# Performance work log

Measured on AMD Instinct MI355X. Metric: run time of the kernel, lower is better.

## Reference

```python
import jax, jax.numpy as jnp
import numpy as np

D = 1024          # feature dim (x_dim)
C = 32            # n classes (way)
SHOTS = 32
N_SUP = C * SHOTS
Q = 1024
REG = 0.5         # reg_param


def setup_inputs() -> dict:
    key = jax.random.key(0)
    ks = jax.random.split(key, 5)
    support_x = jax.random.normal(ks[0], (N_SUP, D), dtype=jnp.float32)
    query_x = jax.random.normal(ks[1], (Q, D), dtype=jnp.float32)
    labels_idx = (jnp.arange(N_SUP, dtype=jnp.int32) % C)  # every class present, equal shots
    m = jax.random.normal(ks[2], (1, D), dtype=jnp.float32) * 0.01
    kappa = jnp.float32(0.1)
    nu = jnp.float32(D)
    triu_diag = jnp.ones((D,), dtype=jnp.float32)
    triu_lower = jnp.eye(D, dtype=jnp.float32) + 0.01 * jax.random.normal(ks[3], (D, D), dtype=jnp.float32)
    return {"support_x": support_x, "query_x": query_x, "labels_idx": labels_idx,
            "m": m, "kappa": kappa, "nu": nu,
            "triu_diag": triu_diag, "triu_lower": triu_lower}


def _metaqda_fb(support_x, query_x, labels_idx, m, kappa, nu, triu_diag, triu_lower):
    onehot = jax.nn.one_hot(labels_idx, C, dtype=support_x.dtype)      # [N, C]
    Nj = jnp.sum(onehot, axis=0)                                       # [C]
    kappa_ = jnp.abs(kappa) + 1e-6
    nu_ = jnp.maximum(nu, jnp.float32(D - 1 + 1e-6))

    # Cholesky-factor prior scatter matrix: L @ L^T
    lower_mask = jnp.tril(jnp.ones((D, D), dtype=support_x.dtype), k=-1)
    L = jnp.diag(jnp.abs(triu_diag)) + triu_lower * lower_mask
    prior_S = L @ L.T                                                  # [D, D]

    # per-class sums (replaces python loop of rank-1 outer products with GEMMs)
    sum_x = onehot.T @ support_x                                       # [C, D]
    mean_x = sum_x / Nj[:, None]
    # sum_n x x^T per class: contract through [N,C,D] intermediate
    SXX = jnp.einsum('nc,nd,ne->cde', onehot, support_x, support_x)    # [C, D, D]

    kN = kappa_ + Nj                                                   # [C]
    mu = (kappa_ / kN)[:, None] * m + (Nj / kN)[:, None] * mean_x      # [C, D]

    mm = m.T @ m                                                       # [D, D]  (self_outer of [1,D])
    mumu = jnp.einsum('cd,ce->cde', mu, mu)                            # [C, D, D]
    S = prior_S[None] + SXX + kappa_ * mm[None] - kN[:, None, None] * mumu

    scale = (kN + 1.0) / ((nu_ + Nj - D + 1.0) * kN)                   # [C]
    sigma = S * scale[:, None, None]                                   # [C, D, D]

    sigma_inv = (1.0 - REG) * jnp.linalg.inv(sigma) + REG * jnp.eye(D, dtype=sigma.dtype)

    common = nu_ + Nj + 1.0 - D                                        # [C]
    _, logdet = jnp.linalg.slogdet(sigma)
    bias = (jax.lax.lgamma(0.5 * (common + D)) - jax.lax.lgamma(0.5 * common)
            - 0.5 * D * jnp.log(common) - 0.5 * logdet)                # [C]

    diff = query_x[:, None, :] - mu[None, :, :]                        # [Q, C, D]
    dist = jnp.einsum('qcd,cde,qce->qc', diff, sigma_inv, diff)        # [Q, C]
    preds = bias[None, :] - 0.5 * (common + D)[None, :] * jnp.log1p(dist / common[None, :])
    return preds


def reference(support_x, query_x, labels_idx, m, kappa, nu, triu_diag, triu_lower):
    return _metaqda_fb(support_x, query_x, labels_idx, m, kappa, nu, triu_diag, triu_lower)
```

## Files before the change

### kernel.cpp

```cpp
#include <hip/hip_runtime.h>
#include <math.h>

#define Dk 1024
#define Ck 32
#define Nk 1024
#define Qk 1024
#define REGP 0.5f
#define NB 64
#define NROWSV (Qk + Nk + Ck + 1)

#define CO_KAPPA 0
#define CO_NU    1
#define CO_NJ    2
#define CO_KN    34
#define CO_SCALE 66
#define CO_COMMON 98
#define CO_COEF  130
#define CO_BIASA 162
#define CO_BIASF 200

#define O_P    0u
#define O_W    2162688u
#define O_T    3211264u
#define O_MU   3473408u
#define O_QM   3506176u
#define O_MB   3538944u
#define O_MI   3578112u
#define O_QNY  3617280u
#define O_QNO  3618304u
#define O_MUN  3619328u
#define O_GMM  3619360u
#define O_EX   3619392u
#define O_CONS 3619408u
#define O_CIDX 3619664u
#define O_YH   3652432u
#define O_YM   4733776u
#define O_YL   5815120u
#define O_WH   6896464u
#define O_WM   7420752u
#define O_WL   7945040u
#define O_OH   8469328u
#define O_OM   9550672u
#define O_OL   10632016u

#define WS_DECL \
    float* P     = Wbuf + O_P;    (void)P; \
    float* W     = Wbuf + O_W;    (void)W; \
    float* Tb    = Wbuf + O_T;    (void)Tb; \
    float* QM    = Wbuf + O_QM;   (void)QM; \
    float* Mbuf  = Wbuf + O_MB;   (void)Mbuf; \
    float* Minv  = Wbuf + O_MI;   (void)Minv; \
    float* qny   = Wbuf + O_QNY;  (void)qny; \
    float* qno   = Wbuf + O_QNO;  (void)qno; \
    float* mun2o = Wbuf + O_MUN;  (void)mun2o; \
    float* gmm   = Wbuf + O_GMM;  (void)gmm; \
    float* extraf= Wbuf + O_EX;   (void)extraf; \
    float* cons  = Wbuf + O_CONS; (void)cons; \
    int*   cidx  = (int*)(Wbuf + O_CIDX); (void)cidx; \
    ushort* sYh = (ushort*)(Wbuf + O_YH); (void)sYh; \
    ushort* sYm = (ushort*)(Wbuf + O_YM); (void)sYm; \
    ushort* sYl = (ushort*)(Wbuf + O_YL); (void)sYl; \
    ushort* sWh = (ushort*)(Wbuf + O_WH); (void)sWh; \
    ushort* sWm = (ushort*)(Wbuf + O_WM); (void)sWm; \
    ushort* sWl = (ushort*)(Wbuf + O_WL); (void)sWl; \
    ushort* sOh = (ushort*)(Wbuf + O_OH); (void)sOh; \
    ushort* sOm = (ushort*)(Wbuf + O_OM); (void)sOm; \
    ushort* sOl = (ushort*)(Wbuf + O_OL); (void)sOl;

typedef __attribute__((ext_vector_type(8))) __bf16 bf16x8;
typedef __attribute__((ext_vector_type(4))) float f32x4;

#define MFMA(a, b, c) __builtin_amdgcn_mfma_f32_16x16x32_bf16(a, b, c, 0, 0, 0)

__device__ __forceinline__ ushort f2bf(float x) {
    unsigned u = __float_as_uint(x);
    return (ushort)((u + 0x7FFFu + ((u >> 16) & 1u)) >> 16);
}
__device__ __forceinline__ float bf2f(ushort h) {
    return __uint_as_float(((unsigned)h) << 16);
}
__device__ __forceinline__ void split1(float x, ushort& h, ushort& m, ushort& l) {
    h = f2bf(x);
    float r1 = x - bf2f(h);
    m = f2bf(r1);
    l = f2bf(r1 - bf2f(m));
}
__device__ __forceinline__ void split_store4(ushort* ph, ushort* pm, ushort* pl,
                                             size_t o, float4 v) {
    float vv[4] = {v.x, v.y, v.z, v.w};
    ushort4 H, M, L;
    ushort* Hp = (ushort*)&H; ushort* Mp = (ushort*)&M; ushort* Lp = (ushort*)&L;
#pragma unroll
    for (int c = 0; c < 4; ++c) split1(vv[c], Hp[c], Mp[c], Lp[c]);
    *(ushort4*)(ph + o) = H;
    *(ushort4*)(pm + o) = M;
    *(ushort4*)(pl + o) = L;
}

__device__ __forceinline__ float wave_red(float s) {
#pragma unroll
    for (int o = 32; o > 0; o >>= 1) s += __shfl_down(s, o, 64);
    return s;
}

#define LDSA(c, r, k8) ((c) * 5120 + (r) * 40 + (k8))
#define LDSB(c, r, k8) (15360 + (c) * 2560 + (r) * 40 + (k8))
#define LDS_HW 23040

__device__ __forceinline__ void tile_fetch8(
    bf16x8* ra, bf16x8* rb,
    const ushort* Ah, const ushort* Am, const ushort* Al, int aRow0, int aRowMax,
    const ushort* Bh, const ushort* Bm, const ushort* Bl, int bRow0,
    int kcol, int t)
{
    bf16x8 z = {};
    int row = t >> 2, kg = t & 3;
#pragma unroll
    for (int u = 0; u < 3; ++u) {
        const ushort* As = (u == 0) ? Ah : ((u == 1) ? Am : Al);
        int gr = aRow0 + row;
        ra[u] = (gr < aRowMax) ? *(const bf16x8*)(As + (size_t)gr * 1024 + kcol + kg * 8) : z;
    }
#pragma unroll
    for (int u = 0; u < 2; ++u) {
        int slot = t + u * 512;
        if (slot < 768) {
            int comp = slot >> 8, rem = slot & 255;
            int br = rem >> 2, bkg = rem & 3;
            const ushort* Bs = (comp == 0) ? Bh : ((comp == 1) ? Bm : Bl);
            rb[u] = *(const bf16x8*)(Bs + (size_t)(bRow0 + br) * 1024 + kcol + bkg * 8);
        }
    }
}

__device__ __forceinline__ void tile_store8(ushort* lds, const bf16x8* ra, const bf16x8* rb, int t) {
    int row = t >> 2, kg = t & 3;
#pragma unroll
    for (int u = 0; u < 3; ++u)
        *(bf16x8*)(lds + LDSA(u, row, kg * 8)) = ra[u];
#pragma unroll
    for (int u = 0; u < 2; ++u) {
        int slot = t + u * 512;
        if (slot < 768) {
            int comp = slot >> 8, rem = slot & 255;
            int br = rem >> 2, bkg = rem & 3;
            *(bf16x8*)(lds + LDSB(comp, br, bkg * 8)) = rb[u];
        }
    }
}

__device__ __forceinline__ void tile_compute8(const ushort* lds, f32x4 acc[4],
                                              int w, int lr, int lk) {
    bf16x8 af[3], bf_[4][3];
#pragma unroll
    for (int c = 0; c < 3; ++c)
        af[c] = *(const bf16x8*)(lds + LDSA(c, w * 16 + lr, lk * 8));
#pragma unroll
    for (int cf = 0; cf < 4; ++cf)
#pragma unroll
        for (int c = 0; c < 3; ++c)
            bf_[cf][c] = *(const bf16x8*)(lds + LDSB(c, cf * 16 + lr, lk * 8));
#pragma unroll
    for (int cf = 0; cf < 4; ++cf) {
        f32x4 a = acc[cf];
        a = MFMA(af[0], bf_[cf][0], a);
        a = MFMA(af[0], bf_[cf][1], a);
        a = MFMA(af[1], bf_[cf][0], a);
        a = MFMA(af[0], bf_[cf][2], a);
        a = MFMA(af[2], bf_[cf][0], a);
        a = MFMA(af[1], bf_[cf][1], a);
        acc[cf] = a;
    }
}

__device__ __forceinline__ void tile_gemm8(
    ushort* lds, f32x4 acc[4],
    const ushort* Ah, const ushort* Am, const ushort* Al, int aRow0, int aRowMax,
    const ushort* Bh, const ushort* Bm, const ushort* Bl, int bRow0,
    int kbase, int ksteps, int t)
{
    const int w = t >> 6, lr = t & 15, lk = (t >> 4) & 3;
    bf16x8 ra[3], rb[2];
    tile_fetch8(ra, rb, Ah, Am, Al, aRow0, aRowMax, Bh, Bm, Bl, bRow0, kbase * 32, t);
    tile_store8(lds, ra, rb, t);
    __syncthreads();
    for (int kt = 0; kt < ksteps; ++kt) {
        if (kt + 1 < ksteps)
            tile_fetch8(ra, rb, Ah, Am, Al, aRow0, aRowMax, Bh, Bm, Bl, bRow0,
                        (kbase + kt + 1) * 32, t);
        tile_compute8(lds, acc, w, lr, lk);
        __syncthreads();
        if (kt + 1 < ksteps)
            tile_store8(lds, ra, rb, t);
        __syncthreads();
    }
}

__device__ __forceinline__ void fetch4(float4* reg, const float* src, int ld,
                                       int rowbase, int rowmax, int colbase, int t) {
#pragma unroll
    for (int u = 0; u < 4; ++u) {
        int slot = t + u * 256;
        int r = slot >> 4, c4 = slot & 15;
        int gr = rowbase + r;
        reg[u] = (gr < rowmax) ? *(const float4*)(src + (size_t)gr * ld + colbase + c4 * 4)
                               : make_float4(0.f, 0.f, 0.f, 0.f);
    }
}
__device__ __forceinline__ void stT(float* dst, const float4* reg, int t) {
#pragma unroll
    for (int u = 0; u < 4; ++u) {
        int slot = t + u * 256;
        int r = slot >> 4, c4 = slot & 15;
        dst[(c4 * 4 + 0) * 68 + r] = reg[u].x;
        dst[(c4 * 4 + 1) * 68 + r] = reg[u].y;
        dst[(c4 * 4 + 2) * 68 + r] = reg[u].z;
        dst[(c4 * 4 + 3) * 68 + r] = reg[u].w;
    }
}
__device__ __forceinline__ void stN(float* dst, const float4* reg, int t) {
#pragma unroll
    for (int u = 0; u < 4; ++u) {
        int slot = t + u * 256;
        int r = slot >> 4, c4 = slot & 15;
        *(float4*)(dst + r * 68 + c4 * 4) = reg[u];
    }
}
__device__ __forceinline__ void gemm16(const float* At, const float* Bt,
                                       float acc[4][4], int tx, int ty) {
#pragma unroll 4
    for (int kk = 0; kk < NB; ++kk) {
        float4 a = *(const float4*)(At + kk * 68 + ty * 4);
        float4 b = *(const float4*)(Bt + kk * 68 + tx * 4);
        float av[4] = {a.x, a.y, a.z, a.w};
        float bv[4] = {b.x, b.y, b.z, b.w};
#pragma unroll
        for (int r = 0; r < 4; ++r)
#pragma unroll
            for (int s = 0; s < 4; ++s) acc[r][s] += av[r] * bv[s];
    }
}
__device__ __forceinline__ void mm_task(
    const float* aSrc, int aLd, int aRow, int aRowMax, int aCol, int aRowStep, int aColStep,
    const float* bSrc, int bLd, int bRow, int bRowMax, int bCol, int bRowStep, int bColStep,
    bool bTrans, int k0, int k1,
    float acc[4][4], float* smA, float* smB, int t, int tx, int ty)
{
    float4 ra[4], rb[4];
    fetch4(ra, aSrc, aLd, aRow + k0 * aRowStep, aRowMax, aCol + k0 * aColStep, t);
    fetch4(rb, bSrc, bLd, bRow + k0 * bRowStep, bRowMax, bCol + k0 * bColStep, t);
    stT(smA, ra, t);
    if (bTrans) stT(smB, rb, t); else stN(smB, rb, t);
    __syncthreads();
    for (int kt = k0; kt < k1; ++kt) {
        if (kt + 1 < k1) {
            fetch4(ra, aSrc, aLd, aRow + (kt + 1) * aRowStep, aRowMax, aCol + (kt + 1) * aColStep, t);
            fetch4(rb, bSrc, bLd, bRow + (kt + 1) * bRowStep, bRowMax, bCol + (kt + 1) * bColStep, t);
        }
        gemm16(smA, smB, acc, tx, ty);
        __syncthreads();
        if (kt + 1 < k1) {
            stT(smA, ra, t);
            if (bTrans) stT(smB, rb, t); else stN(smB, rb, t);
        }
        __syncthreads();
    }
}

__global__ __launch_bounds__(256) void k_p0(const float* qx, const int* labels,
                                            const float* mvec, const float* kappa,
                                            const float* nu, const float* td,
                                            const float* tl, float* Wbuf) {
    __shared__ __align__(16) float smem[9216];
    float* smA = smem;
    float* sX  = smem + 8704;
    WS_DECL
    const int t = threadIdx.x;
    const int lane = t & 63, wv = t >> 6;
    const int tau = blockIdx.x;

    if (tau == 0) {
        int* scnt = (int*)sX;
        if (t < Ck) scnt[t] = 0;
        __syncthreads();
        for (int n = t; n < Nk; n += 256) {
            int l = labels[n];
            int pos = atomicAdd(&scnt[l], 1);
            cidx[l * Nk + pos] = n;
        }
        __syncthreads();
        if (t < Ck) {
            float kap = fabsf(kappa[0]) + 1e-6f;
            float nu_ = fmaxf(nu[0], (float)(Dk - 1) + 1e-6f);
            float Njf = (float)scnt[t];
            float kN = kap + Njf;
            if (t == 0) { cons[CO_KAPPA] = kap; cons[CO_NU] = nu_; }
            cons[CO_NJ + t] = Njf;
            cons[CO_KN + t] = kN;
            cons[CO_SCALE + t] = (kN + 1.0f) / ((nu_ + Njf - (float)Dk + 1.0f) * kN);
            float common = nu_ + Njf + 1.0f - (float)Dk;
            cons[CO_COMMON + t] = common;
            cons[CO_COEF + t] = 0.5f * (common + (float)Dk);
            cons[CO_BIASA + t] = lgammaf(0.5f * (common + (float)Dk)) - lgammaf(0.5f * common)
                                 - 0.5f * (float)Dk * logf(common);
        }
    } else if (tau == 1) {
        float s = 0.f;
        for (int i = t; i < Dk; i += 256) s += logf(fabsf(td[i]));
        s = wave_red(s);
        if (lane == 0) sX[wv] = s;
        __syncthreads();
        if (t == 0) extraf[0] = 2.f * (sX[0] + sX[1] + sX[2] + sX[3]);
    } else if (tau < 18) {
        int b0 = (tau - 2) * NB;
        for (int idx = t; idx < 64 * 64; idx += 256) {
            int m = idx >> 6, i = idx & 63;
            smem[i * 72 + m] = (m > i) ? tl[(size_t)(b0 + m) * Dk + b0 + i] : 0.f;
        }
        if (t < 64) smem[4608 + t] = 1.f / fabsf(td[b0 + t]);
        __syncthreads();
        if (t < 64) {
            const int j = t;
            float r[64];
#pragma unroll
            for (int m = 0; m < 64; ++m) r[m] = (m == j) ? 1.f : 0.f;
#pragma unroll
            for (int i = 0; i < 64; ++i) {
                float x = r[i] * smem[4608 + i];
                r[i] = x;
#pragma unroll
                for (int g = (i >> 2); g < 16; ++g) {
                    float4 lt = *(const float4*)&smem[i * 72 + g * 4];
                    r[g * 4 + 0] -= lt.x * x;
                    r[g * 4 + 1] -= lt.y * x;
                    r[g * 4 + 2] -= lt.z * x;
                    r[g * 4 + 3] -= lt.w * x;
                }
            }
#pragma unroll
            for (int i = 0; i < 64; ++i)
                W[(size_t)(b0 + i) * Dk + b0 + j] = r[i];
        }
    } else if (tau < 21) {
        int base = (tau - 18) * 13056;
        for (int i = t; i < 13056 && base + i < 39168; i += 256) Mbuf[base + i] = 0.f;
    } else if (tau == 21) {
        if (t < 32) { mun2o[t] = 0.f; gmm[t] = 0.f; }
    } else if (tau < 86) {
        int rbase = (tau - 22) * 16;
        for (int j = wv; j < 16; j += 4) {
            const float* row = qx + (size_t)(rbase + j) * Dk;
            float s = 0.f;
            for (int d = lane; d < Dk; d += 64) { float v = row[d]; s += v * v; }
            s = wave_red(s);
            if (lane == 0) qno[rbase + j] = s;
        }
    } else if (tau < 150) {
        int rbase = (tau - 86) * 16;
        for (int j = 0; j < 16; ++j) {
            int r = rbase + j;
            float4 v = ((const float4*)(qx + (size_t)r * Dk))[t];
            split_store4(sYh, sYm, sYl, (size_t)r * 1024 + (size_t)t * 4, v);
        }
    } else if (tau == 150) {
        float4 v = ((const float4*)mvec)[t];
        split_store4(sYh, sYm, sYl, (size_t)2080 * 1024 + (size_t)t * 4, v);
    } else {
        int rbase = (tau - 151) * 16;
        for (int j = 0; j < 16; ++j)
            ((float4*)(P + (size_t)(rbase + j) * 1024))[t] = make_float4(0, 0, 0, 0);
    }
}

__global__ __launch_bounds__(256) void k_p1(const float* sx, const float* mvec, float* Wbuf) {
    __shared__ float sX[512];
    WS_DECL
    const int t = threadIdx.x;
    const int lane = t & 63, wv = t >> 6;
    const int tau = blockIdx.x;
    if (tau < 128) {
        int c = tau >> 2;
        int d = ((tau & 3) << 8) + t;
        int Nj = (int)cons[CO_NJ + c];
        float kap = cons[CO_KAPPA], kN = cons[CO_KN + c];
        float acc = 0.f;
        for (int s = 0; s < Nj; ++s) acc += sx[(size_t)cidx[c * Nk + s] * Dk + d];
        float muv = (kap * mvec[d] + acc) / kN;
        size_t o = (size_t)(2048 + c) * 1024 + d;
        ushort h, m_, l_;
        split1(muv, h, m_, l_);
        sYh[o] = h; sYm[o] = m_; sYl[o] = l_;
        float s2 = wave_red(muv * muv);
        if (lane == 0) sX[wv] = s2;
        __syncthreads();
        if (t == 0) atomicAdd(&mun2o[c], sX[0] + sX[1] + sX[2] + sX[3]);
    } else {
        int rbase = (tau - 128) * 16;
        for (int j = 0; j < 16; ++j) {
            int n = rbase + j;
            int srcrow = cidx[(n >> 5) * Nk + (n & 31)];
            float4 v = ((const float4*)(sx + (size_t)srcrow * Dk))[t];
            split_store4(sYh, sYm, sYl, (size_t)(1024 + n) * 1024 + (size_t)t * 4, v);
        }
    }
}

__global__ __launch_bounds__(256) void k_t1(const float* tl, float* Wbuf) {
    __shared__ __align__(16) float smem[8704];
    float* smA = smem;
    float* smB = smem + 4352;
    WS_DECL
    const int t = threadIdx.x;
    const int tx = t & 15, ty = t >> 4;
    const int BIG = 1 << 30;
    int pb = blockIdx.x * 128;
    float acc[4][4] = {};
    mm_task(tl, Dk, pb + 64, BIG, pb, 0, NB,
            W, Dk, pb, BIG, pb, NB, 0, false, 0, 1,
            acc, smA, smB, t, tx, ty);
    {
        float4 ra[4];
        fetch4(ra, W, Dk, pb + 64, BIG, pb + 64, t);
#pragma unroll
        for (int r = 0; r < 4; ++r)
#pragma unroll
            for (int s = 0; s < 4; ++s)
                smB[(ty * 4 + r) * 68 + tx * 4 + s] = acc[r][s];
        stT(smA, ra, t);
    }
    __syncthreads();
    float acc2[4][4] = {};
    gemm16(smA, smB, acc2, tx, ty);
    __syncthreads();
#pragma unroll
    for (int r = 0; r < 4; ++r)
#pragma unroll
        for (int s = 0; s < 4; ++s)
            W[(size_t)(pb + 64 + ty * 4 + r) * Dk + pb + tx * 4 + s] = -acc2[r][s];
}

__global__ __launch_bounds__(256) void k_tr_a(const float* tl, float* Wbuf, int h, int ht) {
    __shared__ __align__(16) float smem[8704];
    float* smA = smem;
    float* smB = smem + 4352;
    WS_DECL
    const int t = threadIdx.x;
    const int tx = t & 15, ty = t >> 4;
    const int BIG = 1 << 30;
    int tau = blockIdx.x;
    int p = tau / (ht * ht), rr = tau % (ht * ht);
    int i = rr / ht, j = rr % ht;
    int pb = p * 2 * h;
    float acc[4][4] = {};
    mm_task(tl, Dk, pb + h + i * NB, BIG, pb, 0, NB,
            W, Dk, pb, BIG, pb + j * NB, NB, 0, false, 0, ht,
            acc, smA, smB, t, tx, ty);
    float* Tp = Tb + (size_t)p * h * h;
#pragma unroll
    for (int r = 0; r < 4; ++r)
#pragma unroll
        for (int s = 0; s < 4; ++s)
            Tp[(size_t)(i * NB + ty * 4 + r) * h + j * NB + tx * 4 + s] = acc[r][s];
}

__global__ __launch_bounds__(256) void k_tr_b(float* Wbuf, int h, int ht) {
    __shared__ __align__(16) float smem[8704];
    float* smA = smem;
    float* smB = smem + 4352;
    WS_DECL
    const int t = threadIdx.x;
    const int tx = t & 15, ty = t >> 4;
    const int BIG = 1 << 30;
    int tau = blockIdx.x;
    int p = tau / (ht * ht), rr = tau % (ht * ht);
    int i = rr / ht, j = rr % ht;
    int pb = p * 2 * h;
    const float* Tp = Tb + (size_t)p * h * h;
    float acc[4][4] = {};
    mm_task(W, Dk, pb + h + i * NB, BIG, pb + h, 0, NB,
            Tp, h, 0, BIG, j * NB, NB, 0, false, 0, ht,
            acc, smA, smB, t, tx, ty);
#pragma unroll
    for (int r = 0; r < 4; ++r)
#pragma unroll
        for (int s = 0; s < 4; ++s)
            W[(size_t)(pb + h + i * NB + ty * 4 + r) * Dk + pb + j * NB + tx * 4 + s] = -acc[r][s];
}

__global__ __launch_bounds__(256) void k_cvtw(float* Wbuf) {
    WS_DECL
    const int t = threadIdx.x;
#pragma unroll
    for (int u = 0; u < 4; ++u) {
        unsigned g = blockIdx.x * 1024u + u * 256u + t;
        float4 v = ((const float4*)W)[g];
        split_store4(sWh, sWm, sWl, (size_t)g * 4, v);
    }
}

__global__ __launch_bounds__(512) void k_yg(float* Wbuf) {
    __shared__ __align__(16) ushort lds[LDS_HW];
    WS_DECL
    const int t = threadIdx.x;
    int b = blockIdx.x;
    int s = (b & 7) * 34 + (b >> 3);
    int jt = 15 - s / 17, rt = s % 17;
    f32x4 acc[4] = {};
    tile_gemm8(lds, acc, sYh, sYm, sYl, rt * 128, 2081,
               sWh, sWm, sWl, jt * 64, 0, (jt + 1) * 2, t);
    const int w = t >> 6, lr = t & 15, lk = (t >> 4) & 3;
#pragma unroll
    for (int cf = 0; cf < 4; ++cf)
#pragma unroll
        for (int r = 0; r < 4; ++r) {
            int grow = rt * 128 + w * 16 + lk * 4 + r;
            if (grow < NROWSV) {
                size_t o = (size_t)grow * 1024 + jt * 64 + cf * 16 + lr;
                ushort h, m_, l_;
                split1(acc[cf][r], h, m_, l_);
                sOh[o] = h; sOm[o] = m_; sOl[o] = l_;
            }
        }
}

__global__ __launch_bounds__(512) void k_p4m(float* Wbuf) {
    __shared__ __align__(16) ushort lds[LDS_HW];
    WS_DECL
    const int t = threadIdx.x;
    int b = blockIdx.x;
    int s = (b & 7) * 74 + (b >> 3);
    const int w = t >> 6, lr = t & 15, lk = (t >> 4) & 3;
    f32x4 acc[4] = {};
    if (s < 576) {
        int qt = s / 36, rem = s % 36;
        int mt = rem >> 2, kc = rem & 3;
        tile_gemm8(lds, acc, sOh, sOm, sOl, 1024 + mt * 128, 2081,
                   sOh, sOm, sOl, qt * 64, kc * 8, 8, t);
#pragma unroll
        for (int cf = 0; cf < 4; ++cf)
#pragma unroll
            for (int r = 0; r < 4; ++r) {
                int n = mt * 128 + w * 16 + lk * 4 + r;
                if (n < Nk + Ck + 1)
                    atomicAdd(&P[(size_t)n * 1024 + qt * 64 + cf * 16 + lr], acc[cf][r]);
            }
    } else {
        int qt = s - 576;
        tile_gemm8(lds, acc, sYh, sYm, sYl, 2048, 2081,
                   sYh, sYm, sYl, qt * 64, 0, 32, t);
#pragma unroll
        for (int cf = 0; cf < 4; ++cf)
#pragma unroll
            for (int r = 0; r < 4; ++r) {
                int rq = w * 16 + lk * 4 + r;
                if (rq < 32)
                    QM[(size_t)rq * 1024 + qt * 64 + cf * 16 + lr] = acc[cf][r];
            }
    }
}

__global__ __launch_bounds__(256) void k_gram(float* Wbuf) {
    __shared__ __align__(16) float smA[34 * 68];
    WS_DECL
    const int t = threadIdx.x;
    const int lane = t & 63, wv = t >> 6;
    const int tau = blockIdx.x;
    if (tau < 128) {
        int c = tau >> 2, kc = tau & 3;
        float accg[5];
        int iu[5], ju[5];
#pragma unroll
        for (int u = 0; u < 5; ++u) {
            int e = t + u * 256;
            iu[u] = e / 34; ju[u] = e - iu[u] * 34;
            accg[u] = 0.f;
        }
        for (int kt = kc * 4; kt < kc * 4 + 4; ++kt) {
            for (int e2 = t; e2 < 34 * NB; e2 += 256) {
                int i = e2 >> 6, k = e2 & 63;
                int yr = (i < 32) ? (Qk + c * 32 + i) : ((i == 32) ? (Qk + Nk + c) : (Qk + Nk + Ck));
                size_t o = (size_t)yr * 1024 + kt * NB + k;
                smA[i * 68 + k] = bf2f(sOh[o]) + bf2f(sOm[o]) + bf2f(sOl[o]);
            }
            __syncthreads();
#pragma unroll
            for (int u = 0; u < 5; ++u) {
                int e = t + u * 256;
                if (e < 1156) {
                    float s = 0.f;
                    for (int k = 0; k < NB; ++k) s += smA[iu[u] * 68 + k] * smA[ju[u] * 68 + k];
                    accg[u] += s;
                }
            }
            __syncthreads();
        }
#pragma unroll
        for (int u = 0; u < 5; ++u) {
            int e = t + u * 256;
            if (e < 1156)
                atomicAdd(&Mbuf[c * 1224 + iu[u] * 36 + ju[u]], accg[u]);
        }
    } else {
        int rbase = (tau - 128) * 16;
        for (int j = wv; j < 16; j += 4) {
            size_t ro = (size_t)(rbase + j) * 1024;
            float s = 0.f;
            for (int d = lane; d < Dk; d += 64) {
                size_t o = ro + d;
                float v = bf2f(sOh[o]) + bf2f(sOm[o]) + bf2f(sOl[o]);
                s += v * v;
            }
            s = wave_red(s);
            if (lane == 0) qny[rbase + j] = s;
        }
    }
}

__global__ __launch_bounds__(256) void k_p5(float* Wbuf) {
    __shared__ float smem[2464];
    float* Ml = smem;
    float* Z  = smem + 1200;
    float* Dv = smem + 2400;
    WS_DECL
    const int t = threadIdx.x;
    const int c = blockIdx.x;
    float kN = cons[CO_KN + c], kap = cons[CO_KAPPA];
    for (int e = t; e < 34 * 34; e += 256) {
        int i = e / 34, j = e - i * 34;
        Ml[i * 35 + j] = Mbuf[c * 1224 + i * 36 + j];
    }
    __syncthreads();
    if (t == 0) {
        gmm[c] = Ml[32 * 35 + 32];
        Ml[32 * 35 + 32] += -1.f / kN;
        Ml[33 * 35 + 33] += 1.f / kap;
    }
    if (t < 32) Ml[t * 35 + t] += 1.f;
    __syncthreads();
    for (int j = 0; j < 34; ++j) {
        if (t == 0) {
            float s = Ml[j * 35 + j];
            for (int k = 0; k < j; ++k) s -= Ml[j * 35 + k] * Ml[j * 35 + k] * Dv[k];
            Dv[j] = s;
        }
        __syncthreads();
        if (t > j && t < 34) {
            float s = Ml[t * 35 + j];
            for (int k = 0; k < j; ++k) s -= Ml[t * 35 + k] * Ml[j * 35 + k] * Dv[k];
            Ml[t * 35 + j] = s / Dv[j];
        }
        __syncthreads();
    }
    if (t < 34) {
        for (int i = 0; i < 34; ++i) {
            float s = (i == t) ? 1.f : 0.f;
            for (int k = 0; k < i; ++k) s -= Ml[i * 35 + k] * Z[k * 35 + t];
            Z[i * 35 + t] = s;
        }
        for (int i = 33; i >= 0; --i) {
            float s = Z[i * 35 + t] / Dv[i];
            for (int k = i + 1; k < 34; ++k) s -= Ml[k * 35 + i] * Z[k * 35 + t];
            Z[i * 35 + t] = s;
        }
    }
    __syncthreads();
    for (int e = t; e < 34 * 34; e += 256) {
        int i = e / 34, j = e - i * 34;
        Minv[c * 1224 + i * 36 + j] = Z[i * 35 + j];
    }
    if (t == 0) {
        float ld = 0.f;
        for (int j = 0; j < 34; ++j) ld += logf(fabsf(Dv[j]));
        float scale = cons[CO_SCALE + c];
        float logdet = (float)Dk * logf(scale) + extraf[0] + logf(kN) + logf(kap) + ld;
        cons[CO_BIASF + c] = cons[CO_BIASA + c] - 0.5f * logdet;
    }
}

__global__ __launch_bounds__(256) void k_p6(float* Wbuf, float* out) {
    __shared__ __align__(16) float smem[3904];
    float* Mi  = smem;
    float* wL  = smem + 1200;
    float* gsm = smem + 3520;
    float* red = smem + 3520 + 128;
    WS_DECL
    const int t = threadIdx.x;
    const int tau = blockIdx.x;
    int qt = tau >> 5, c = tau & 31;
    for (int e = t; e < 34 * 34; e += 256) {
        int i = e / 34, j = e - i * 34;
        Mi[i * 35 + j] = Minv[c * 1224 + i * 36 + j];
    }
    if (t < 34)
        gsm[t] = (t < 32) ? Mbuf[c * 1224 + t * 36 + 32]
                          : ((t == 32) ? gmm[c] : Mbuf[c * 1224 + 33 * 36 + 32]);
    __syncthreads();
    for (int e = t; e < 34 * NB; e += 256) {
        int i = e >> 6, qq = e & 63;
        int prow = (i < 32) ? (c * 32 + i) : ((i == 32) ? (Nk + c) : (Nk + Ck));
        wL[i * 68 + qq] = P[(size_t)prow * Qk + qt * NB + qq] - gsm[i];
    }
    __syncthreads();
    {
        int q = t & 63, part = t >> 6;
        int start = (part < 2) ? part * 9 : 18 + (part - 2) * 8;
        int cnt = (part < 2) ? 9 : 8;
        float partial = 0.f;
        for (int i = start; i < start + cnt; ++i) {
            float v = 0.f;
            for (int j = 0; j < 34; ++j) v += Mi[i * 35 + j] * wL[j * 68 + q];
            partial += v * wL[i * 68 + q];
        }
        red[part * 64 + q] = partial;
    }
    __syncthreads();
    if (t < 64) {
        int q = t;
        float quad = red[q] + red[64 + q] + red[128 + q] + red[192 + q];
        int qg = qt * NB + q;
        float w32 = wL[32 * 68 + q];
        float ydist2 = qny[qg] - 2.f * w32 - gmm[c];
        float dd = qno[qg] + mun2o[c] - 2.f * QM[(size_t)c * Qk + qg];
        float scale = cons[CO_SCALE + c], common = cons[CO_COMMON + c];
        float dist = (1.f - REGP) / scale * (ydist2 - quad) + REGP * dd;
        out[(size_t)qg * Ck + c] = cons[CO_BIASF + c] - cons[CO_COEF + c] * log1pf(dist / common);
    }
}

extern "C" void kernel_launch(void* const* d_in, const int* in_sizes, int n_in,
                              void* d_out, int out_size, void* d_ws, size_t ws_size,
                              hipStream_t stream) {
    const float* sx = (const float*)d_in[0];
    const float* qx = (const float*)d_in[1];
    const int* labels = (const int*)d_in[2];
    const float* mvec = (const float*)d_in[3];
    const float* kappa = (const float*)d_in[4];
    const float* nu = (const float*)d_in[5];
    const float* td = (const float*)d_in[6];
    const float* tl = (const float*)d_in[7];
    float* W = (float*)d_ws;
    float* out = (float*)d_out;

    hipLaunchKernelGGL(k_p0, dim3(219), dim3(256), 0, stream,
                       qx, labels, mvec, kappa, nu, td, tl, W);
    hipLaunchKernelGGL(k_p1, dim3(192), dim3(256), 0, stream, sx, mvec, W);
    hipLaunchKernelGGL(k_t1, dim3(8), dim3(256), 0, stream, tl, W);
    for (int l = 2; l <= 4; ++l) {
        int h = 32 << l, ht = h >> 6, pairs = 16 >> l;
        int nt = pairs * ht * ht;
        hipLaunchKernelGGL(k_tr_a, dim3(nt), dim3(256), 0, stream, tl, W, h, ht);
        hipLaunchKernelGGL(k_tr_b, dim3(nt), dim3(256), 0, stream, W, h, ht);
    }
    hipLaunchKernelGGL(k_cvtw, dim3(256), dim3(256), 0, stream, W);
    hipLaunchKernelGGL(k_yg, dim3(272), dim3(512), 0, stream, W);
    hipLaunchKernelGGL(k_p4m, dim3(592), dim3(512), 0, stream, W);
    hipLaunchKernelGGL(k_gram, dim3(192), dim3(256), 0, stream, W);
    hipLaunchKernelGGL(k_p5, dim3(32), dim3(256), 0, stream, W);
    hipLaunchKernelGGL(k_p6, dim3(512), dim3(256), 0, stream, W, out);
}
```

Before: 412.1 us.

## Use 128x128 split-bf16 MFMA tiles with split-K atomics for Y and P GEMMs

```diff
diff --git a/kernel.cpp b/kernel.cpp
--- a/kernel.cpp
+++ b/kernel.cpp
@@ -104,94 +104,86 @@
 }
 
 #define LDSA(c, r, k8) ((c) * 5120 + (r) * 40 + (k8))
-#define LDSB(c, r, k8) (15360 + (c) * 2560 + (r) * 40 + (k8))
-#define LDS_HW 23040
-
-__device__ __forceinline__ void tile_fetch8(
+#define LDSB(c, r, k8) (15360 + (c) * 5120 + (r) * 40 + (k8))
+#define LDS_HW 30720
+
+__device__ __forceinline__ void tile_fetch2(
     bf16x8* ra, bf16x8* rb,
     const ushort* Ah, const ushort* Am, const ushort* Al, int aRow0, int aRowMax,
     const ushort* Bh, const ushort* Bm, const ushort* Bl, int bRow0,
     int kcol, int t)
 {
     bf16x8 z = {};
-    int row = t >> 2, kg = t & 3;
-#pragma unroll
-    for (int u = 0; u < 3; ++u) {
-        const ushort* As = (u == 0) ? Ah : ((u == 1) ? Am : Al);
+#pragma unroll
+    for (int u = 0; u < 6; ++u) {
+        int comp = u >> 1;
+        int idx = ((u & 1) << 8) + t;
+        int row = idx >> 2, kg = idx & 3;
+        const ushort* As = (comp == 0) ? Ah : ((comp == 1) ? Am : Al);
         int gr = aRow0 + row;
         ra[u] = (gr < aRowMax) ? *(const bf16x8*)(As + (size_t)gr * 1024 + kcol + kg * 8) : z;
-    }
-#pragma unroll
-    for (int u = 0; u < 2; ++u) {
-        int slot = t + u * 512;
-        if (slot < 768) {
-            int comp = slot >> 8, rem = slot & 255;
-            int br = rem >> 2, bkg = rem & 3;
-            const ushort* Bs = (comp == 0) ? Bh : ((comp == 1) ? Bm : Bl);
-            rb[u] = *(const bf16x8*)(Bs + (size_t)(bRow0 + br) * 1024 + kcol + bkg * 8);
-        }
-    }
-}
-
-__device__ __forceinline__ void tile_store8(ushort* lds, const bf16x8* ra, const bf16x8* rb, int t) {
-    int row = t >> 2, kg = t & 3;
-#pragma unroll
-    for (int u = 0; u < 3; ++u)
-        *(bf16x8*)(lds + LDSA(u, row, kg * 8)) = ra[u];
-#pragma unroll
-    for (int u = 0; u < 2; ++u) {
-        int slot = t + u * 512;
-        if (slot < 768) {
-            int comp = slot >> 8, rem = slot & 255;
-            int br = rem >> 2, bkg = rem & 3;
-            *(bf16x8*)(lds + LDSB(comp, br, bkg * 8)) = rb[u];
-        }
-    }
-}
-
-__device__ __forceinline__ void tile_compute8(const ushort* lds, f32x4 acc[4],
+        const ushort* Bs = (comp == 0) ? Bh : ((comp == 1) ? Bm : Bl);
+        rb[u] = *(const bf16x8*)(Bs + (size_t)(bRow0 + row) * 1024 + kcol + kg * 8);
+    }
+}
+
+__device__ __forceinline__ void tile_store2(ushort* lds, const bf16x8* ra, const bf16x8* rb, int t) {
+#pragma unroll
+    for (int u = 0; u < 6; ++u) {
+        int comp = u >> 1;
+        int idx = ((u & 1) << 8) + t;
+        int row = idx >> 2, kg = idx & 3;
+        *(bf16x8*)(lds + LDSA(comp, row, kg * 8)) = ra[u];
+        *(bf16x8*)(lds + LDSB(comp, row, kg * 8)) = rb[u];
+    }
+}
+
+__device__ __forceinline__ void tile_compute2(const ushort* lds, f32x4 acc[2][8],
                                               int w, int lr, int lk) {
-    bf16x8 af[3], bf_[4][3];
-#pragma unroll
-    for (int c = 0; c < 3; ++c)
-        af[c] = *(const bf16x8*)(lds + LDSA(c, w * 16 + lr, lk * 8));
-#pragma unroll
-    for (int cf = 0; cf < 4; ++cf)
+    bf16x8 af[2][3];
+#pragma unroll
+    for (int rf = 0; rf < 2; ++rf)
 #pragma unroll
         for (int c = 0; c < 3; ++c)
-            bf_[cf][c] = *(const bf16x8*)(lds + LDSB(c, cf * 16 + lr, lk * 8));
-#pragma unroll
-    for (int cf = 0; cf < 4; ++cf) {
-        f32x4 a = acc[cf];
-        a = MFMA(af[0], bf_[cf][0], a);
-        a = MFMA(af[0], bf_[cf][1], a);
-        a = MFMA(af[1], bf_[cf][0], a);
-        a = MFMA(af[0], bf_[cf][2], a);
-        a = MFMA(af[2], bf_[cf][0], a);
-        a = MFMA(af[1], bf_[cf][1], a);
-        acc[cf] = a;
-    }
-}
-
-__device__ __forceinline__ void tile_gemm8(
-    ushort* lds, f32x4 acc[4],
+            af[rf][c] = *(const bf16x8*)(lds + LDSA(c, w * 32 + rf * 16 + lr, lk * 8));
+#pragma unroll
+    for (int cf = 0; cf < 8; ++cf) {
+        bf16x8 bh = *(const bf16x8*)(lds + LDSB(0, cf * 16 + lr, lk * 8));
+        bf16x8 bm = *(const bf16x8*)(lds + LDSB(1, cf * 16 + lr, lk * 8));
+        bf16x8 bl = *(const bf16x8*)(lds + LDSB(2, cf * 16 + lr, lk * 8));
+#pragma unroll
+        for (int rf = 0; rf < 2; ++rf) {
+            f32x4 a = acc[rf][cf];
+            a = MFMA(af[rf][0], bh, a);
+            a = MFMA(af[rf][0], bm, a);
+            a = MFMA(af[rf][1], bh, a);
+            a = MFMA(af[rf][0], bl, a);
+            a = MFMA(af[rf][2], bh, a);
+            a = MFMA(af[rf][1], bm, a);
+            acc[rf][cf] = a;
+        }
+    }
+}
+
+__device__ __forceinline__ void tile_gemm2(
+    ushort* lds, f32x4 acc[2][8],
     const ushort* Ah, const ushort* Am, const ushort* Al, int aRow0, int aRowMax,
     const ushort* Bh, const ushort* Bm, const ushort* Bl, int bRow0,
     int kbase, int ksteps, int t)
 {
     const int w = t >> 6, lr = t & 15, lk = (t >> 4) & 3;
-    bf16x8 ra[3], rb[2];
-    tile_fetch8(ra, rb, Ah, Am, Al, aRow0, aRowMax, Bh, Bm, Bl, bRow0, kbase * 32, t);
-    tile_store8(lds, ra, rb, t);
+    bf16x8 ra[6], rb[6];
+    tile_fetch2(ra, rb, Ah, Am, Al, aRow0, aRowMax, Bh, Bm, Bl, bRow0, kbase * 32, t);
+    tile_store2(lds, ra, rb, t);
     __syncthreads();
     for (int kt = 0; kt < ksteps; ++kt) {
         if (kt + 1 < ksteps)
-            tile_fetch8(ra, rb, Ah, Am, Al, aRow0, aRowMax, Bh, Bm, Bl, bRow0,
+            tile_fetch2(ra, rb, Ah, Am, Al, aRow0, aRowMax, Bh, Bm, Bl, bRow0,
                         (kbase + kt + 1) * 32, t);
-        tile_compute8(lds, acc, w, lr, lk);
+        tile_compute2(lds, acc, w, lr, lk);
         __syncthreads();
         if (kt + 1 < ksteps)
-            tile_store8(lds, ra, rb, t);
+            tile_store2(lds, ra, rb, t);
         __syncthreads();
     }
 }
@@ -275,6 +267,7 @@
     float* smA = smem;
     float* sX  = smem + 8704;
     WS_DECL
+    float* Yo32 = Wbuf;
     const int t = threadIdx.x;
     const int lane = t & 63, wv = t >> 6;
     const int tau = blockIdx.x;
@@ -346,6 +339,8 @@
         for (int i = t; i < 13056 && base + i < 39168; i += 256) Mbuf[base + i] = 0.f;
     } else if (tau == 21) {
         if (t < 32) { mun2o[t] = 0.f; gmm[t] = 0.f; }
+        for (int i = t; i < 8192; i += 256)
+            ((float4*)QM)[i] = make_float4(0, 0, 0, 0);
     } else if (tau < 86) {
         int rbase = (tau - 22) * 16;
         for (int j = wv; j < 16; j += 4) {
@@ -368,7 +363,7 @@
     } else {
         int rbase = (tau - 151) * 16;
         for (int j = 0; j < 16; ++j)
-            ((float4*)(P + (size_t)(rbase + j) * 1024))[t] = make_float4(0, 0, 0, 0);
+            ((float4*)(Yo32 + (size_t)(rbase + j) * 1024))[t] = make_float4(0, 0, 0, 0);
     }
 }
 
@@ -493,69 +488,107 @@
 #pragma unroll
     for (int u = 0; u < 4; ++u) {
         unsigned g = blockIdx.x * 1024u + u * 256u + t;
+        int row = g >> 8, col4 = (g & 255) * 4;
         float4 v = ((const float4*)W)[g];
+        if (col4 + 0 > row) v.x = 0.f;
+        if (col4 + 1 > row) v.y = 0.f;
+        if (col4 + 2 > row) v.z = 0.f;
+        if (col4 + 3 > row) v.w = 0.f;
         split_store4(sWh, sWm, sWl, (size_t)g * 4, v);
     }
 }
 
-__global__ __launch_bounds__(512) void k_yg(float* Wbuf) {
+__global__ __launch_bounds__(256) void k_yg(float* Wbuf) {
     __shared__ __align__(16) ushort lds[LDS_HW];
     WS_DECL
-    const int t = threadIdx.x;
-    int b = blockIdx.x;
-    int s = (b & 7) * 34 + (b >> 3);
-    int jt = 15 - s / 17, rt = s % 17;
-    f32x4 acc[4] = {};
-    tile_gemm8(lds, acc, sYh, sYm, sYl, rt * 128, 2081,
-               sWh, sWm, sWl, jt * 64, 0, (jt + 1) * 2, t);
+    float* Yo32 = Wbuf;
+    const int t = threadIdx.x;
+    int e = blockIdx.x;
+    int q = e / 17, rt = e % 17;
+    int jt2, kc;
+    if (q < 4)       { jt2 = 7; kc = q; }
+    else if (q < 8)  { jt2 = 6; kc = q - 4; }
+    else if (q < 11) { jt2 = 5; kc = q - 8; }
+    else if (q < 14) { jt2 = 4; kc = q - 11; }
+    else if (q < 16) { jt2 = 3; kc = q - 14; }
+    else if (q < 18) { jt2 = 2; kc = q - 16; }
+    else if (q == 18){ jt2 = 1; kc = 0; }
+    else             { jt2 = 0; kc = 0; }
+    int ksteps = min(8, 4 * (jt2 + 1) - kc * 8);
+    f32x4 acc[2][8] = {};
+    tile_gemm2(lds, acc, sYh, sYm, sYl, rt * 128, 2081,
+               sWh, sWm, sWl, jt2 * 128, kc * 8, ksteps, t);
     const int w = t >> 6, lr = t & 15, lk = (t >> 4) & 3;
 #pragma unroll
-    for (int cf = 0; cf < 4; ++cf)
-#pragma unroll
-        for (int r = 0; r < 4; ++r) {
-            int grow = rt * 128 + w * 16 + lk * 4 + r;
-            if (grow < NROWSV) {
-                size_t o = (size_t)grow * 1024 + jt * 64 + cf * 16 + lr;
-                ushort h, m_, l_;
-                split1(acc[cf][r], h, m_, l_);
-                sOh[o] = h; sOm[o] = m_; sOl[o] = l_;
+    for (int rf = 0; rf < 2; ++rf)
+#pragma unroll
+        for (int cf = 0; cf < 8; ++cf)
+#pragma unroll
+            for (int r = 0; r < 4; ++r) {
+                int grow = rt * 128 + w * 32 + rf * 16 + lk * 4 + r;
+                if (grow < NROWSV)
+                    atomicAdd(&Yo32[(size_t)grow * 1024 + jt2 * 128 + cf * 16 + lr],
+                              acc[rf][cf][r]);
             }
-        }
-}
-
-__global__ __launch_bounds__(512) void k_p4m(float* Wbuf) {
+}
+
+__global__ __launch_bounds__(256) void k_cvto(float* Wbuf) {
+    WS_DECL
+    float* Yo32 = Wbuf;
+    const int t = threadIdx.x;
+    int rbase = blockIdx.x * 4;
+#pragma unroll
+    for (int j = 0; j < 4; ++j) {
+        int r = rbase + j;
+        float4 v = ((const float4*)(Yo32 + (size_t)r * 1024))[t];
+        split_store4(sOh, sOm, sOl, (size_t)r * 1024 + (size_t)t * 4, v);
+    }
+    if (rbase < 1088) {
+#pragma unroll
+        for (int j = 0; j < 4; ++j)
+            ((float4*)(Yo32 + (size_t)(rbase + j) * 1024))[t] = make_float4(0, 0, 0, 0);
+    }
+}
+
+__global__ __launch_bounds__(256) void k_p4m(float* Wbuf) {
     __shared__ __align__(16) ushort lds[LDS_HW];
     WS_DECL
     const int t = threadIdx.x;
-    int b = blockIdx.x;
-    int s = (b & 7) * 74 + (b >> 3);
+    int e = blockIdx.x;
     const int w = t >> 6, lr = t & 15, lk = (t >> 4) & 3;
-    f32x4 acc[4] = {};
-    if (s < 576) {
-        int qt = s / 36, rem = s % 36;
-        int mt = rem >> 2, kc = rem & 3;
-        tile_gemm8(lds, acc, sOh, sOm, sOl, 1024 + mt * 128, 2081,
-                   sOh, sOm, sOl, qt * 64, kc * 8, 8, t);
-#pragma unroll
-        for (int cf = 0; cf < 4; ++cf)
-#pragma unroll
-            for (int r = 0; r < 4; ++r) {
-                int n = mt * 128 + w * 16 + lk * 4 + r;
-                if (n < Nk + Ck + 1)
-                    atomicAdd(&P[(size_t)n * 1024 + qt * 64 + cf * 16 + lr], acc[cf][r]);
-            }
+    f32x4 acc[2][8] = {};
+    if (e < 288) {
+        int tile = e >> 2, kc = e & 3;
+        int mt = tile >> 3, qt2 = tile & 7;
+        tile_gemm2(lds, acc, sOh, sOm, sOl, 1024 + mt * 128, 2081,
+                   sOh, sOm, sOl, qt2 * 128, kc * 8, 8, t);
+#pragma unroll
+        for (int rf = 0; rf < 2; ++rf)
+#pragma unroll
+            for (int cf = 0; cf < 8; ++cf)
+#pragma unroll
+                for (int r = 0; r < 4; ++r) {
+                    int n = mt * 128 + w * 32 + rf * 16 + lk * 4 + r;
+                    if (n < Nk + Ck + 1)
+                        atomicAdd(&P[(size_t)n * 1024 + qt2 * 128 + cf * 16 + lr],
+                                  acc[rf][cf][r]);
+                }
     } else {
-        int qt = s - 576;
-        tile_gemm8(lds, acc, sYh, sYm, sYl, 2048, 2081,
-                   sYh, sYm, sYl, qt * 64, 0, 32, t);
-#pragma unroll
-        for (int cf = 0; cf < 4; ++cf)
-#pragma unroll
-            for (int r = 0; r < 4; ++r) {
-                int rq = w * 16 + lk * 4 + r;
-                if (rq < 32)
-                    QM[(size_t)rq * 1024 + qt * 64 + cf * 16 + lr] = acc[cf][r];
-            }
+        int f = e - 288;
+        int qt2 = f >> 2, kc = f & 3;
+        tile_gemm2(lds, acc, sYh, sYm, sYl, 2048, 2080,
+                   sYh, sYm, sYl, qt2 * 128, kc * 8, 8, t);
+#pragma unroll
+        for (int rf = 0; rf < 2; ++rf)
+#pragma unroll
+            for (int cf = 0; cf < 8; ++cf)
+#pragma unroll
+                for (int r = 0; r < 4; ++r) {
+                    int rq = w * 32 + rf * 16 + lk * 4 + r;
+                    if (rq < 32)
+                        atomicAdd(&QM[(size_t)rq * 1024 + qt2 * 128 + cf * 16 + lr],
+                                  acc[rf][cf][r]);
+                }
     }
 }
 
@@ -741,7 +774,7 @@
     float* W = (float*)d_ws;
     float* out = (float*)d_out;
 
-    hipLaunchKernelGGL(k_p0, dim3(219), dim3(256), 0, stream,
+    hipLaunchKernelGGL(k_p0, dim3(283), dim3(256), 0, stream,
                        qx, labels, mvec, kappa, nu, td, tl, W);
     hipLaunchKernelGGL(k_p1, dim3(192), dim3(256), 0, stream, sx, mvec, W);
     hipLaunchKernelGGL(k_t1, dim3(8), dim3(256), 0, stream, tl, W);
@@ -752,8 +785,9 @@
         hipLaunchKernelGGL(k_tr_b, dim3(nt), dim3(256), 0, stream, W, h, ht);
     }
     hipLaunchKernelGGL(k_cvtw, dim3(256), dim3(256), 0, stream, W);
-    hipLaunchKernelGGL(k_yg, dim3(272), dim3(512), 0, stream, W);
-    hipLaunchKernelGGL(k_p4m, dim3(592), dim3(512), 0, stream, W);
+    hipLaunchKernelGGL(k_yg, dim3(340), dim3(256), 0, stream, W);
+    hipLaunchKernelGGL(k_cvto, dim3(528), dim3(256), 0, stream, W);
+    hipLaunchKernelGGL(k_p4m, dim3(320), dim3(256), 0, stream, W);
     hipLaunchKernelGGL(k_gram, dim3(192), dim3(256), 0, stream, W);
     hipLaunchKernelGGL(k_p5, dim3(32), dim3(256), 0, stream, W);
     hipLaunchKernelGGL(k_p6, dim3(512), dim3(256), 0, stream, W, out);
```

New measurement: 369.9 us. 1.11x faster.
